# Kernel optimization log

Measured on AMD Instinct MI355X. Metric: run time of the kernel, lower is better.

Reference implementation:

```python
import jax, jax.numpy as jnp
import numpy as np

B, T, F_IN, N, H = 16, 2048, 64, 24, 64  # batch, time, input_dim, num_nodes, hidden_dim
ALPHA = 0.2        # LeakyReLU negative slope
NEG_INF = -9e15    # mask value used by the torch module


def setup_inputs() -> dict:
    key = jax.random.key(0)
    k0, k1, k2, k3, k4 = jax.random.split(key, 5)
    x = jax.random.normal(k0, (B, T, F_IN), dtype=jnp.float32)
    adj = jax.random.randint(k1, (N, N), 0, 2, dtype=jnp.int32)  # binary adjacency
    # input_projector: Linear(input_dim, num_nodes*hidden_dim)
    Wp = jax.random.normal(k2, (F_IN, N * H), dtype=jnp.float32) * 0.05
    bp = jnp.zeros((N * H,), dtype=jnp.float32)
    # GraphAttentionLayer params: W (in=H, out=H), a (2H, 1)
    W = jax.random.normal(k3, (H, H), dtype=jnp.float32) * 0.05
    a = jax.random.normal(k4, (2 * H, 1), dtype=jnp.float32) * 0.05
    return {"x": x, "adj": adj, "Wp": Wp, "bp": bp, "W": W, "a": a}


def reference(x, adj, Wp, bp, W, a):
    Bx, Tx, Fx = x.shape
    BT = Bx * Tx
    # input projector -> per-node features (BT, N, H)
    h = (x.reshape(BT, Fx) @ Wp + bp).reshape(BT, N, H)
    # GAT layer (concat=True), eval mode so dropout is identity
    Wh = h @ W  # (BT, N, H)
    # e[b,i,j] = LeakyReLU([Wh_i ; Wh_j] @ a) = LeakyReLU(Wh_i@a1 + Wh_j@a2)
    a1, a2 = a[:H, 0], a[H:, 0]
    f1 = Wh @ a1  # (BT, N)
    f2 = Wh @ a2  # (BT, N)
    e = f1[:, :, None] + f2[:, None, :]
    e = jnp.where(e > 0, e, ALPHA * e)
    e = jnp.where(adj[None, :, :] > 0, e, jnp.float32(NEG_INF))
    attn = jax.nn.softmax(e, axis=2)  # (BT, N, N)
    h_prime = jnp.einsum('bij,bjh->bih', attn, Wh)  # (BT, N, H)
    h_prime = jax.nn.elu(h_prime)
    out = h_prime.mean(axis=1)  # mean over nodes -> (BT, H)
    return out.reshape(Bx, Tx, H)
```

## Files before the change

### kernel.cpp

```cpp
#include <hip/hip_runtime.h>
#include <hip/hip_bf16.h>

#define F_IN   64
#define NN     24
#define HH     64
#define CC     1536
#define CCX    1584
#define NTILE  99
#define ROWS   16
#define BT_TOT (16 * 2048)
#define ALPHA_ 0.2f
#define NEG_INF_ -9.0e15f
#define LOG2E_ 1.4426950408889634f
#define ATS    24

typedef short bf16x8 __attribute__((ext_vector_type(8)));
typedef float f32x4  __attribute__((ext_vector_type(4)));

#if defined(__has_builtin)
#  if __has_builtin(__builtin_amdgcn_cvt_pk_bf16_f32)
#    define HAS_PK_BF16 1
#  endif
#  if __has_builtin(__builtin_amdgcn_exp2f)
#    define HAS_EXP2 1
#  endif
#  if __has_builtin(__builtin_amdgcn_rcpf)
#    define HAS_RCP 1
#  endif
#  if __has_builtin(__builtin_amdgcn_fmed3f)
#    define HAS_MED3 1
#  endif
#endif
#ifndef HAS_PK_BF16
#  define HAS_PK_BF16 0
#endif
#ifndef HAS_EXP2
#  define HAS_EXP2 0
#endif
#ifndef HAS_RCP
#  define HAS_RCP 0
#endif
#ifndef HAS_MED3
#  define HAS_MED3 0
#endif

__device__ __forceinline__ short f2bf(float f) {
    unsigned u = __float_as_uint(f);
    return (short)((u + 0x7FFFu + ((u >> 16) & 1u)) >> 16);
}

__device__ __forceinline__ int pk2bf(float a, float b) {
#if HAS_PK_BF16
    typedef __bf16 bfv2 __attribute__((ext_vector_type(2)));
    bfv2 r = __builtin_amdgcn_cvt_pk_bf16_f32(a, b);
    return __builtin_bit_cast(int, r);
#else
    return (int)(unsigned short)f2bf(a) | ((int)f2bf(b) << 16);
#endif
}

__device__ __forceinline__ float exp2_fast(float x) {
#if HAS_EXP2
    return __builtin_amdgcn_exp2f(x);
#else
    return __expf(0.6931471805599453f * x);
#endif
}

__device__ __forceinline__ float rcp_fast(float x) {
#if HAS_RCP
    return __builtin_amdgcn_rcpf(x);
#else
    return 1.0f / x;
#endif
}

__device__ __forceinline__ float elu_fast(float v) {
#if HAS_MED3
    return __builtin_amdgcn_fmed3f(v, exp2_fast(v * LOG2E_) - 1.f, 0.f);
#else
    return (v > 0.f) ? v : (exp2_fast(v * LOG2E_) - 1.f);
#endif
}

__device__ __forceinline__ bf16x8 pk8bf(float4 lo, float4 hi) {
    int4 r;
    r.x = pk2bf(lo.x, lo.y);
    r.y = pk2bf(lo.z, lo.w);
    r.z = pk2bf(hi.x, hi.y);
    r.w = pk2bf(hi.z, hi.w);
    return __builtin_bit_cast(bf16x8, r);
}

__global__ __launch_bounds__(256) void precompute_kernel(
    const float* __restrict__ Wp,
    const float* __restrict__ bp,
    const float* __restrict__ W,
    const float* __restrict__ a,
    const int*   __restrict__ adj,
    short* __restrict__ Bpk,
    float* __restrict__ bpWx,
    float* __restrict__ maskf)
{
    __shared__ float WpS[64 * 65];
    __shared__ float WS[64 * 17];
    __shared__ float Wa[128];
    const int b = blockIdx.x, tid = threadIdx.x;

    if (b < 96) {
        const int n64 = (b >> 2) * 64;
        const int jc0 = (b & 3) * 16;
        for (int i = tid; i < 4096; i += 256)
            WpS[(i >> 6) * 65 + (i & 63)] = Wp[(size_t)(i >> 6) * CC + n64 + (i & 63)];
        for (int i = tid; i < 1024; i += 256)
            WS[(i >> 4) * 17 + (i & 15)] = W[(i >> 4) * 64 + jc0 + (i & 15)];
        __syncthreads();

        const int k = tid & 63, q0 = (tid >> 6) * 4;
        float acc[4] = {0.f, 0.f, 0.f, 0.f};
        #pragma unroll 4
        for (int m = 0; m < 64; ++m) {
            const float wp = WpS[k * 65 + m];
            #pragma unroll
            for (int j = 0; j < 4; ++j)
                acc[j] += wp * WS[m * 17 + q0 + j];
        }
        const int s2 = k >> 5, jj = k & 7, lbase = ((k >> 3) & 3) * 16;
        #pragma unroll
        for (int j = 0; j < 4; ++j) {
            const int l = lbase + q0 + j;
            Bpk[((size_t)(b * 2 + s2) * 64 + l) * 8 + jj] = f2bf(acc[j]);
        }
    } else {
        const bool needWa = (b < 108) || (b == 114);
        if (needWa) {
            if (tid < 128) {
                const int which = tid >> 6, m = tid & 63;
                float s = 0.f;
                #pragma unroll 8
                for (int h = 0; h < 64; ++h)
                    s += W[m * 64 + h] * a[which * 64 + h];
                Wa[tid] = s;
            }
            __syncthreads();
        }
        if (b < 108) {
            const int u  = (b - 96) * 256 + tid;
            const int jj = u & 7, l = (u >> 3) & 63, s2 = (u >> 9) & 1, te = u >> 10;
            const int t  = 96 + te;
            const int k  = s2 * 32 + ((l >> 4) << 3) + jj;
            const int ff = te * 16 + (l & 15);
            const int which = (ff >= NN) ? 1 : 0;
            const int node  = ff - which * NN;
            float v = 0.f;
            #pragma unroll 8
            for (int m = 0; m < 64; ++m)
                v += Wp[(size_t)k * CC + node * 64 + m] * Wa[which * 64 + m];
            Bpk[((size_t)(t * 2 + s2) * 64 + l) * 8 + jj] = f2bf(v * LOG2E_);
        } else {
            const int c = (b - 108) * 256 + tid;
            if (c < CC) {
                const int n = c >> 6, jc = c & 63;
                float s = 0.f;
                #pragma unroll 8
                for (int m = 0; m < 64; ++m) s += bp[n * 64 + m] * W[m * 64 + jc];
                bpWx[c] = s;
            } else if (c < CCX) {
                const int ff = c - CC;
                const int which = (ff >= NN) ? 1 : 0;
                const int node  = ff - which * NN;
                float s = 0.f;
                #pragma unroll 8
                for (int m = 0; m < 64; ++m) s += bp[node * 64 + m] * Wa[which * 64 + m];
                bpWx[c] = s * LOG2E_;
            }
            if (b == 114) {
                for (int i = tid; i < NN * NN; i += 256)
                    maskf[i] = (adj[i] > 0) ? 0.f : NEG_INF_;
            }
        }
    }
}

__global__ __launch_bounds__(1024, 8) void gat_main_kernel(
    const float* __restrict__ x,
    const float* __restrict__ maskf,
    const short* __restrict__ Bpk,
    const float* __restrict__ bpWx,
    float* __restrict__ out)
{
    __shared__ __align__(16) short whB[ROWS * 4 * 48 * 8];
    __shared__ __align__(16) short attn16[ROWS * NN * ATS];
    __shared__ __align__(16) short zero16[8];
    __shared__ __align__(16) float maskQ[6 * 24 * 4];
    __shared__ float fs[ROWS * 48];

    const int tid  = threadIdx.x;
    const int lane = tid & 63;
    const int wid  = tid >> 6;
    const int quad = lane >> 4;
    const int lm   = lane & 15;
    const size_t base = (size_t)blockIdx.x * ROWS;

    const float* xr = x + (base + lm) * F_IN + quad * 8;
    const float4 xa = *(const float4*)(xr);
    const float4 xb = *(const float4*)(xr + 4);
    const float4 xc = *(const float4*)(xr + 32);
    const float4 xd = *(const float4*)(xr + 36);

    if (tid < 8) zero16[tid] = 0;
    if (tid < NN * NN) {
        const int i = tid / NN, rem = tid - i * NN;
        const int gg = (rem >= 12) ? 1 : 0;
        const int jl = rem - gg * 12;
        const int q = jl >> 2, c = jl & 3;
        maskQ[((gg * 3 + q) * NN + i) * 4 + c] = maskf[tid];
    }

    {
        const bf16x8 a0 = pk8bf(xa, xb);
        const bf16x8 a1 = pk8bf(xc, xd);

        if (wid < 12) {
            const int g  = wid >> 2;
            const int nt = wid & 3;
            short* wb0 = whB + ((nt * 48 + g * 16 + lm) * 8) + quad * 4 * 1536;
            int pA[4], pB[4];
            {
                f32x4 acc[4];
                #pragma unroll
                for (int k = 0; k < 4; ++k) {
                    const int t = (g * 8 + k) * 4 + nt;
                    const short* bq = Bpk + ((size_t)(t * 2) * 64 + lane) * 8;
                    const bf16x8 b0 = *(const bf16x8*)bq;
                    const bf16x8 b1 = *(const bf16x8*)(bq + 512);
                    const float bb = bpWx[t * 16 + lm];
                    f32x4 c = {bb, bb, bb, bb};
                    c = __builtin_amdgcn_mfma_f32_16x16x32_bf16(a0, b0, c, 0, 0, 0);
                    c = __builtin_amdgcn_mfma_f32_16x16x32_bf16(a1, b1, c, 0, 0, 0);
                    acc[k] = c;
                }
                #pragma unroll
                for (int i = 0; i < 4; ++i) {
                    pA[i] = pk2bf(acc[0][i], acc[1][i]);
                    pB[i] = pk2bf(acc[2][i], acc[3][i]);
                }
            }
            {
                f32x4 acc[4];
                #pragma unroll
                for (int k = 0; k < 4; ++k) {
                    const int t = (g * 8 + 4 + k) * 4 + nt;
                    const short* bq = Bpk + ((size_t)(t * 2) * 64 + lane) * 8;
                    const bf16x8 b0 = *(const bf16x8*)bq;
                    const bf16x8 b1 = *(const bf16x8*)(bq + 512);
                    const float bb = bpWx[t * 16 + lm];
                    f32x4 c = {bb, bb, bb, bb};
                    c = __builtin_amdgcn_mfma_f32_16x16x32_bf16(a0, b0, c, 0, 0, 0);
                    c = __builtin_amdgcn_mfma_f32_16x16x32_bf16(a1, b1, c, 0, 0, 0);
                    acc[k] = c;
                }
                #pragma unroll
                for (int i = 0; i < 4; ++i) {
                    int4 w;
                    w.x = pA[i];
                    w.y = pB[i];
                    w.z = pk2bf(acc[0][i], acc[1][i]);
                    w.w = pk2bf(acc[2][i], acc[3][i]);
                    *(int4*)(wb0 + i * 1536) = w;
                }
            }
        } else if (wid < 15) {
            const int t = 96 + (wid - 12);
            const short* bq = Bpk + ((size_t)(t * 2) * 64 + lane) * 8;
            const bf16x8 b0 = *(const bf16x8*)bq;
            const bf16x8 b1 = *(const bf16x8*)(bq + 512);
            const float bb = bpWx[t * 16 + lm];
            f32x4 acc = {bb, bb, bb, bb};
            acc = __builtin_amdgcn_mfma_f32_16x16x32_bf16(a0, b0, acc, 0, 0, 0);
            acc = __builtin_amdgcn_mfma_f32_16x16x32_bf16(a1, b1, acc, 0, 0, 0);
            const int ff = (t - 96) * 16 + lm;
            #pragma unroll
            for (int i = 0; i < 4; ++i)
                fs[(quad * 4 + i) * 48 + ff] = acc[i];
        }
    }
    __syncthreads();

    const int r = wid;
    short* attn_r = attn16 + r * NN * ATS;

    const int gg = lane >> 5;
    const int i  = lane & 31;
    const int jb = gg * 12;

    const float f1i = fs[r * 48 + i];
    const int mr = (i < NN) ? i : 0;

    float f2v[12], mrow[12];
    {
        const float* fp = fs + r * 48 + NN + jb;
        const float4 fa = *(const float4*)(fp);
        const float4 fb = *(const float4*)(fp + 4);
        const float4 fc = *(const float4*)(fp + 8);
        f2v[0]=fa.x; f2v[1]=fa.y; f2v[2]=fa.z; f2v[3]=fa.w;
        f2v[4]=fb.x; f2v[5]=fb.y; f2v[6]=fb.z; f2v[7]=fb.w;
        f2v[8]=fc.x; f2v[9]=fc.y; f2v[10]=fc.z; f2v[11]=fc.w;
        const float* mp = maskQ + gg * 288 + mr * 4;
        const float4 ma = *(const float4*)(mp);
        const float4 mb = *(const float4*)(mp + 96);
        const float4 mc = *(const float4*)(mp + 192);
        mrow[0]=ma.x; mrow[1]=ma.y; mrow[2]=ma.z; mrow[3]=ma.w;
        mrow[4]=mb.x; mrow[5]=mb.y; mrow[6]=mb.z; mrow[7]=mb.w;
        mrow[8]=mc.x; mrow[9]=mc.y; mrow[10]=mc.z; mrow[11]=mc.w;
    }

    float ev[12];
    float ssum = 0.f;
    #pragma unroll
    for (int j = 0; j < 12; ++j) {
        float e = f1i + f2v[j];
        e = fmaxf(e, ALPHA_ * e);
        const float p = exp2_fast(e + mrow[j]);
        ev[j] = p;
        ssum += p;
    }
    const float tot = ssum + __shfl_xor(ssum, 32, 64);
    const float inv = rcp_fast(tot);

    if (i < NN) {
        int pq[6];
        #pragma unroll
        for (int q = 0; q < 6; ++q)
            pq[q] = pk2bf(ev[2 * q] * inv, ev[2 * q + 1] * inv);
        short* dst = attn_r + i * ATS + jb;
        if (gg == 0) {
            *(int4*)(dst)     = make_int4(pq[0], pq[1], pq[2], pq[3]);
            *(int2*)(dst + 8) = make_int2(pq[4], pq[5]);
        } else {
            *(int2*)(dst)     = make_int2(pq[0], pq[1]);
            *(int4*)(dst + 4) = make_int4(pq[2], pq[3], pq[4], pq[5]);
        }
    }

    const short* pa0src = (quad < 3) ? (attn_r + lm * ATS + quad * 8) : zero16;
    const short* pa1src = (quad < 3 && lm < 8)
        ? (attn_r + (16 + lm) * ATS + quad * 8) : zero16;
    const bf16x8 pa0 = *(const bf16x8*)pa0src;
    const bf16x8 pa1 = *(const bf16x8*)pa1src;
    #pragma unroll
    for (int ntp = 0; ntp < 4; ++ntp) {
        const short* bsrc = (lane < 48)
            ? (whB + r * 1536 + (ntp * 48 + lane) * 8) : zero16;
        const bf16x8 bw = *(const bf16x8*)bsrc;
        f32x4 c0 = {0.f, 0.f, 0.f, 0.f};
        f32x4 c1 = {0.f, 0.f, 0.f, 0.f};
        __builtin_amdgcn_s_setprio(1);
        c0 = __builtin_amdgcn_mfma_f32_16x16x32_bf16(pa0, bw, c0, 0, 0, 0);
        c1 = __builtin_amdgcn_mfma_f32_16x16x32_bf16(pa1, bw, c1, 0, 0, 0);
        __builtin_amdgcn_s_setprio(0);
        float s = 0.f;
        #pragma unroll
        for (int k = 0; k < 4; ++k)
            s += elu_fast(c0[k]);
        #pragma unroll
        for (int k = 0; k < 4; ++k)
            s += elu_fast(c1[k]);
        s += __shfl_xor(s, 16, 64);
        s += __shfl_xor(s, 32, 64);
        if (quad == 0)
            out[(base + r) * HH + ntp * 16 + lm] = s * (1.0f / 24.0f);
    }
}

extern "C" void kernel_launch(void* const* d_in, const int* in_sizes, int n_in,
                              void* d_out, int out_size, void* d_ws, size_t ws_size,
                              hipStream_t stream)
{
    const float* x   = (const float*)d_in[0];
    const int*   adj = (const int*)d_in[1];
    const float* Wp  = (const float*)d_in[2];
    const float* bp  = (const float*)d_in[3];
    const float* W   = (const float*)d_in[4];
    const float* a   = (const float*)d_in[5];
    float* out = (float*)d_out;

    short* Bpk   = (short*)d_ws;
    float* bpWx  = (float*)(Bpk + (size_t)NTILE * 1024);
    float* maskf = bpWx + CCX;

    precompute_kernel<<<115, 256, 0, stream>>>(Wp, bp, W, a, adj, Bpk, bpWx, maskf);
    gat_main_kernel<<<BT_TOT / ROWS, 1024, 0, stream>>>(x, maskf, Bpk, bpWx, out);
}
```

Measured before the change: 118.0 us.

## Stage x through LDS as bf16, pre-permute mask layout, drop setprio

```diff
diff --git a/kernel.cpp b/kernel.cpp
--- a/kernel.cpp
+++ b/kernel.cpp
@@ -12,6 +12,7 @@
 #define ALPHA_ 0.2f
 #define NEG_INF_ -9.0e15f
 #define LOG2E_ 1.4426950408889634f
+#define XSP    72
 #define ATS    24
 
 typedef short bf16x8 __attribute__((ext_vector_type(8)));
@@ -81,15 +82,6 @@
 #else
     return (v > 0.f) ? v : (exp2_fast(v * LOG2E_) - 1.f);
 #endif
-}
-
-__device__ __forceinline__ bf16x8 pk8bf(float4 lo, float4 hi) {
-    int4 r;
-    r.x = pk2bf(lo.x, lo.y);
-    r.y = pk2bf(lo.z, lo.w);
-    r.z = pk2bf(hi.x, hi.y);
-    r.w = pk2bf(hi.z, hi.w);
-    return __builtin_bit_cast(bf16x8, r);
 }
 
 __global__ __launch_bounds__(256) void precompute_kernel(
@@ -175,8 +167,14 @@
                 bpWx[c] = s * LOG2E_;
             }
             if (b == 114) {
-                for (int i = tid; i < NN * NN; i += 256)
-                    maskf[i] = (adj[i] > 0) ? 0.f : NEG_INF_;
+                for (int u = tid; u < NN * NN; u += 256) {
+                    const int i = u / NN, j = u - i * NN;
+                    const int gg = (j >= 12) ? 1 : 0;
+                    const int jl = j - gg * 12;
+                    const int q = jl >> 2, cc = jl & 3;
+                    maskf[((gg * 3 + q) * NN + i) * 4 + cc] =
+                        (adj[u] > 0) ? 0.f : NEG_INF_;
+                }
             }
         }
     }
@@ -189,6 +187,7 @@
     const float* __restrict__ bpWx,
     float* __restrict__ out)
 {
+    __shared__ __align__(16) short xs16[ROWS * XSP];
     __shared__ __align__(16) short whB[ROWS * 4 * 48 * 8];
     __shared__ __align__(16) short attn16[ROWS * NN * ATS];
     __shared__ __align__(16) short zero16[8];
@@ -202,24 +201,17 @@
     const int lm   = lane & 15;
     const size_t base = (size_t)blockIdx.x * ROWS;
 
-    const float* xr = x + (base + lm) * F_IN + quad * 8;
-    const float4 xa = *(const float4*)(xr);
-    const float4 xb = *(const float4*)(xr + 4);
-    const float4 xc = *(const float4*)(xr + 32);
-    const float4 xd = *(const float4*)(xr + 36);
-
     if (tid < 8) zero16[tid] = 0;
-    if (tid < NN * NN) {
-        const int i = tid / NN, rem = tid - i * NN;
-        const int gg = (rem >= 12) ? 1 : 0;
-        const int jl = rem - gg * 12;
-        const int q = jl >> 2, c = jl & 3;
-        maskQ[((gg * 3 + q) * NN + i) * 4 + c] = maskf[tid];
-    }
-
+    if (tid < NN * NN) maskQ[tid] = maskf[tid];
     {
-        const bf16x8 a0 = pk8bf(xa, xb);
-        const bf16x8 a1 = pk8bf(xc, xd);
+        const int rr = tid >> 6, k = tid & 63;
+        xs16[rr * XSP + k] = f2bf(x[base * F_IN + tid]);
+    }
+    __syncthreads();
+
+    {
+        const bf16x8 a0 = *(const bf16x8*)(xs16 + lm * XSP + quad * 8);
+        const bf16x8 a1 = *(const bf16x8*)(xs16 + lm * XSP + 32 + quad * 8);
 
         if (wid < 12) {
             const int g  = wid >> 2;
@@ -355,10 +347,8 @@
         const bf16x8 bw = *(const bf16x8*)bsrc;
         f32x4 c0 = {0.f, 0.f, 0.f, 0.f};
         f32x4 c1 = {0.f, 0.f, 0.f, 0.f};
-        __builtin_amdgcn_s_setprio(1);
         c0 = __builtin_amdgcn_mfma_f32_16x16x32_bf16(pa0, bw, c0, 0, 0, 0);
         c1 = __builtin_amdgcn_mfma_f32_16x16x32_bf16(pa1, bw, c1, 0, 0, 0);
-        __builtin_amdgcn_s_setprio(0);
         float s = 0.f;
         #pragma unroll
         for (int k = 0; k < 4; ++k)
```

Measured after the change: 108.0 us. 8.4% less time.
